# Kernel optimization log

Measured on AMD Instinct MI355X. Metric: run time of the kernel, lower is better.

The kernel has to match this reference:

```python
import jax, jax.numpy as jnp
import numpy as np
from jax import lax

# norse LIFParameters defaults: dt=1e-3, tau_mem_inv=100, tau_syn_inv=200, v_leak=0, v_reset=0
ALPHA = 100.0
DT_TM = 0.1   # dt * tau_mem_inv
DT_TS = 0.2   # dt * tau_syn_inv

@jax.custom_vjp
def superspike(x):
    # Heaviside forward, SuperSpike surrogate gradient backward
    return (x > 0).astype(x.dtype)

def _ss_fwd(x):
    return superspike(x), x

def _ss_bwd(x, g):
    return (g / (ALPHA * jnp.abs(x) + 1.0) ** 2,)

superspike.defvjp(_ss_fwd, _ss_bwd)

def lif_step(inp, v, i, v_th):
    # norse lif_feed_forward_step (feedforward LIF cell)
    v_dec = v + DT_TM * (i - v)           # v_leak = 0
    i_dec = i * (1.0 - DT_TS)
    z = superspike(v_dec - v_th)
    v_new = (1.0 - z) * v_dec             # reset to v_reset = 0 on spike
    return z, v_new, i_dec + inp

def conv2d(x, w):
    return lax.conv_general_dilated(x, w, (1, 1), 'VALID',
                                    dimension_numbers=('NCHW', 'OIHW', 'NCHW'))

def avg_pool2(x):
    s = lax.reduce_window(x, jnp.zeros((), x.dtype), lax.add,
                          (1, 1, 2, 2), (1, 1, 2, 2), 'VALID')
    return s * jnp.asarray(0.25, x.dtype)

def setup_inputs() -> dict:
    key = jax.random.key(0)
    ks = jax.random.split(key, 6)
    x = jax.random.uniform(ks[0], (40, 256, 1, 28, 28), dtype=jnp.float32)
    # kaiming-ish scales (1/sqrt(fan_in))
    w_conv1 = jax.random.normal(ks[1], (20, 1, 3, 3), jnp.float32) * (1.0 / np.sqrt(9))
    w_conv2 = jax.random.normal(ks[2], (50, 20, 3, 3), jnp.float32) * (1.0 / np.sqrt(180))
    w_fc1 = jax.random.normal(ks[3], (500, 6050), jnp.float32) * (1.0 / np.sqrt(6050))
    w_fc2 = jax.random.normal(ks[4], (200, 500), jnp.float32) * (1.0 / np.sqrt(500))
    w_fc_out = jax.random.normal(ks[5], (10, 200), jnp.float32) * (1.0 / np.sqrt(200))
    return {"x": x, "w_conv1": w_conv1, "w_conv2": w_conv2,
            "w_fc1": w_fc1, "w_fc2": w_fc2, "w_fc_out": w_fc_out}

def reference(x, w_conv1, w_conv2, w_fc1, w_fc2, w_fc_out):
    T, B = x.shape[0], x.shape[1]
    dt = x.dtype
    z0 = jnp.zeros((B, 20, 26, 26), dt)
    z1 = jnp.zeros((B, 50, 11, 11), dt)
    z2 = jnp.zeros((B, 500), dt)
    z3 = jnp.zeros((B, 200), dt)
    zo = jnp.zeros((B, 10), dt)
    carry0 = (z0, z0, z1, z1, z2, z2, z3, z3, zo, zo)

    def step(carry, xt):
        v0, i0, v1, i1, v2, i2, v3, i3, vo, io = carry
        z = conv2d(xt, w_conv1)
        z, v0, i0 = lif_step(z, v0, i0, 0.2)
        z = avg_pool2(z)
        z = conv2d(z, w_conv2)
        z, v1, i1 = lif_step(z, v1, i1, 0.2)
        z = z.reshape(B, -1)                      # [B, 50*11*11]
        z = z @ w_fc1.T
        z, v2, i2 = lif_step(z, v2, i2, 0.1)
        z = z @ w_fc2.T
        z, v3, i3 = lif_step(z, v3, i3, 0.05)
        z = z @ w_fc_out.T
        # LICell (norse li_feed_forward_step): output is decayed membrane voltage
        v_dec = vo + DT_TM * (io - vo)
        i_new = io * (1.0 - DT_TS) + z
        return (v0, i0, v1, i1, v2, i2, v3, i3, v_dec, i_new), v_dec

    _, voltages = lax.scan(step, carry0, x)
    return voltages  # [T, B, output_neurons]
```

## Files before the change

kernel.cpp:

```cpp
#include <hip/hip_runtime.h>
#include <hip/hip_bf16.h>

typedef _Float16 f16x8 __attribute__((ext_vector_type(8)));
typedef float f32x4  __attribute__((ext_vector_type(4)));
typedef unsigned short u16x4 __attribute__((ext_vector_type(4)));

#define T_STEPS 40
#define BATCH   256
#define S2LO    0.000244140625f

__device__ __forceinline__ unsigned short f2h_bits(float f) {
    union { _Float16 h; unsigned short u; } c; c.h = (_Float16)f; return c.u;
}

__device__ __forceinline__ float lif_update(float inp, float& v, float& i, float vth) {
    float vd = __fadd_rn(v, __fmul_rn(0.1f, __fsub_rn(i, v)));
    float id = __fmul_rn(0.8f, i);
    float z  = (vd > vth) ? 1.0f : 0.0f;
    v = (vd > vth) ? 0.0f : vd;
    i = __fadd_rn(id, inp);
    return z;
}

__device__ __forceinline__ void llds16(const unsigned short* g, void* l) {
    __builtin_amdgcn_global_load_lds(
        (const __attribute__((address_space(1))) unsigned int*)g,
        (__attribute__((address_space(3))) unsigned int*)l, 16, 0, 0);
}

__global__ __launch_bounds__(512) void k_conv1(
    const float* __restrict__ x,
    const float* __restrict__ w1,
    unsigned char* __restrict__ s0)
{
    const int b    = blockIdx.y;
    const int tid  = threadIdx.x;
    const int cell = blockIdx.x*512 + tid;
    const bool active = cell < 3380;
    const int pos  = cell / 20;
    const int oc   = cell % 20;
    const int pr   = pos / 13, q = pos % 13;
    const int r0   = 2*pr, c0 = 2*q;

    __shared__ __align__(16) float xl[2][784];

    float wr[9];
    if (active) {
        #pragma unroll
        for (int j = 0; j < 9; ++j) wr[j] = w1[oc*9 + j];
    }
    float vs[2][2], is[2][2];
    #pragma unroll
    for (int dr = 0; dr < 2; ++dr)
        #pragma unroll
        for (int dc = 0; dc < 2; ++dc) { vs[dr][dc] = 0.f; is[dr][dc] = 0.f; }

    if (tid < 196) {
        const float4* xs4 = (const float4*)(x + (size_t)b*784);
        *(float4*)&xl[0][tid*4] = xs4[tid];
    }

    for (int t = 0; t < T_STEPS; ++t) {
        __syncthreads();
        if (t + 1 < T_STEPS && tid < 196) {
            const float4* xs4 = (const float4*)(x + (size_t)((t+1)*BATCH + b)*784);
            *(float4*)&xl[(t+1)&1][tid*4] = xs4[tid];
        }
        const float* xc = xl[t&1];
        size_t base = (size_t)(t*BATCH + b) * 4096;

        if (active) {
            float tle[4][4];
            #pragma unroll
            for (int r = 0; r < 4; ++r) {
                *(float2*)&tle[r][0] = *(const float2*)&xc[(r0 + r)*28 + c0];
                *(float2*)&tle[r][2] = *(const float2*)&xc[(r0 + r)*28 + c0 + 2];
            }
            int zsum = 0;
            #pragma unroll
            for (int dr = 0; dr < 2; ++dr)
                #pragma unroll
                for (int dc = 0; dc < 2; ++dc) {
                    float acc = 0.f;
                    #pragma unroll
                    for (int kr = 0; kr < 3; ++kr)
                        #pragma unroll
                        for (int kc = 0; kc < 3; ++kc)
                            acc += tle[dr+kr][dc+kc] * wr[kr*3+kc];
                    float z = lif_update(acc, vs[dr][dc], is[dr][dc], 0.2f);
                    zsum += (z > 0.5f) ? 1 : 0;
                }
            s0[base + (size_t)pos*24 + oc] = (unsigned char)zsum;
        } else {
            int p2 = cell - 3380;
            for (int idx = p2; idx < 716; idx += 204) {
                if (idx < 676) s0[base + (size_t)(idx >> 2)*24 + 20 + (idx & 3)] = 0;
                else           s0[base + 4056 + (idx - 676)] = 0;
            }
        }
    }
}

__global__ __launch_bounds__(256, 2) void k_conv2(
    const unsigned char* __restrict__ s0,
    const float* __restrict__ w2,
    unsigned short* __restrict__ z1)
{
    const int b    = blockIdx.x >> 1;
    const int half = blockIdx.x & 1;
    const int tid  = threadIdx.x;
    const int wv   = tid >> 6;
    const int lane = tid & 63;
    const int l15  = lane & 15;
    const int kg   = lane >> 4;
    const int wm   = wv;

    __shared__ __align__(16) unsigned short w2h[32*232];
    __shared__ __align__(16) unsigned short w2m[32*232];
    __shared__ __align__(16) unsigned short sIn[2*4096];

    for (int s = tid; s < 32*232; s += 256) {
        int ocw = s / 232, kk = s % 232;
        int g = kk / 24, ic = kk % 24;
        int oc = half*32 + ocw;
        float val = 0.f;
        if (oc < 50 && g < 9 && ic < 20) val = w2[(oc*20 + ic)*9 + g];
        _Float16 h = (_Float16)val;
        float r1 = (val - (float)h) * 4096.0f;
        union { _Float16 h; unsigned short u; } ch, cm;
        ch.h = h; cm.h = (_Float16)r1;
        w2h[s] = ch.u;
        w2m[s] = cm.u;
    }

    int addrA[2][7];
    #pragma unroll
    for (int mt = 0; mt < 2; ++mt) {
        int pos = wm*32 + mt*16 + l15;
        #pragma unroll
        for (int kt = 0; kt < 7; ++kt) {
            int k = kt*32 + kg*8;
            int g = k / 24, o = k - g*24;
            if (pos <= 120 && g <= 8) {
                int in_idx = pos + 2*(pos/11) + 13*(g/3) + (g % 3);
                addrA[mt][kt] = in_idx*48 + o*2;
            } else addrA[mt][kt] = 8128;
        }
    }

    {
        const unsigned char* srow = s0 + (size_t)(0*BATCH + b)*4096;
        uint4 raw = *(const uint4*)(srow + tid*16);
        unsigned short hv[16];
        #pragma unroll
        for (int w = 0; w < 4; ++w) {
            unsigned int u = ((const unsigned int*)&raw)[w];
            #pragma unroll
            for (int j = 0; j < 4; ++j)
                hv[w*4+j] = f2h_bits(0.25f * (float)((u >> (8*j)) & 0xFFu));
        }
        unsigned short* dst = sIn + tid*16;
        *(f16x8*)dst       = *(const f16x8*)&hv[0];
        *(f16x8*)(dst + 8) = *(const f16x8*)&hv[8];
    }
    __syncthreads();

    f16x8 bfrH[2][7], bfrM[2][7];
    #pragma unroll
    for (int nt = 0; nt < 2; ++nt) {
        int n = nt*16 + l15;
        #pragma unroll
        for (int kt = 0; kt < 7; ++kt) {
            bfrH[nt][kt] = *(const f16x8*)&w2h[n*232 + kt*32 + kg*8];
            bfrM[nt][kt] = *(const f16x8*)&w2m[n*232 + kt*32 + kg*8];
        }
    }

    float vst[2][2][4], ist[2][2][4];
    #pragma unroll
    for (int mt = 0; mt < 2; ++mt)
        #pragma unroll
        for (int nt = 0; nt < 2; ++nt)
            #pragma unroll
            for (int r = 0; r < 4; ++r) { vst[mt][nt][r] = 0.f; ist[mt][nt][r] = 0.f; }

    const f32x4 zero4 = {0.f, 0.f, 0.f, 0.f};

    for (int t = 0; t < T_STEPS; ++t) {
        if (t > 0) __syncthreads();

        uint4 raw;
        if (t + 1 < T_STEPS)
            raw = *(const uint4*)(s0 + (size_t)((t+1)*BATCH + b)*4096 + tid*16);

        const char* curB = (const char*)(sIn + (t&1)*4096);

        f32x4 acch[2][2], accl[2][2];
        #pragma unroll
        for (int mt = 0; mt < 2; ++mt)
            #pragma unroll
            for (int nt = 0; nt < 2; ++nt) { acch[mt][nt] = zero4; accl[mt][nt] = zero4; }

        #pragma unroll
        for (int kt = 0; kt < 7; ++kt) {
            #pragma unroll
            for (int mt = 0; mt < 2; ++mt) {
                f16x8 a = *(const f16x8*)(curB + addrA[mt][kt]);
                #pragma unroll
                for (int nt = 0; nt < 2; ++nt) {
                    acch[mt][nt] = __builtin_amdgcn_mfma_f32_16x16x32_f16(
                        a, bfrH[nt][kt], acch[mt][nt], 0, 0, 0);
                    accl[mt][nt] = __builtin_amdgcn_mfma_f32_16x16x32_f16(
                        a, bfrM[nt][kt], accl[mt][nt], 0, 0, 0);
                }
            }
        }

        size_t rowoff = (size_t)(t*BATCH + b) * 6208;
        #pragma unroll
        for (int mt = 0; mt < 2; ++mt) {
            int posb = wm*32 + mt*16 + kg*4;
            #pragma unroll
            for (int nt = 0; nt < 2; ++nt) {
                int ocn = half*32 + nt*16 + l15;
                u16x4 pack;
                #pragma unroll
                for (int r = 0; r < 4; ++r) {
                    float inp = __fadd_rn(acch[mt][nt][r], __fmul_rn(S2LO, accl[mt][nt][r]));
                    float z = lif_update(inp, vst[mt][nt][r], ist[mt][nt][r], 0.2f);
                    int pos = posb + r;
                    pack[r] = (pos <= 120 && z > 0.5f) ? (unsigned short)0x3C00 : (unsigned short)0;
                }
                if (ocn < 50 && posb < 121)
                    *(u16x4*)(z1 + rowoff + ocn*124 + posb) = pack;
            }
        }
        if (half == 0 && tid < 8) z1[rowoff + 6200 + tid] = 0;

        if (t + 1 < T_STEPS) {
            unsigned short hv[16];
            #pragma unroll
            for (int w = 0; w < 4; ++w) {
                unsigned int u = ((const unsigned int*)&raw)[w];
                #pragma unroll
                for (int j = 0; j < 4; ++j)
                    hv[w*4+j] = f2h_bits(0.25f * (float)((u >> (8*j)) & 0xFFu));
            }
            unsigned short* dst = sIn + ((t+1)&1)*4096 + tid*16;
            *(f16x8*)dst       = *(const f16x8*)&hv[0];
            *(f16x8*)(dst + 8) = *(const f16x8*)&hv[8];
        }
    }
}

__global__ __launch_bounds__(256, 3) void k_gemm(
    const unsigned short* __restrict__ A,
    const unsigned short* __restrict__ B0,
    float* __restrict__ C0,
    int Kp, int kiters, int ldc, int nstore,
    size_t strideB, size_t strideC)
{
    __shared__ __align__(16) unsigned short As[128*64];
    __shared__ __align__(16) unsigned short Bs[128*64];
    const unsigned short* B = B0 + (size_t)blockIdx.z * strideB;
    float* C = C0 + (size_t)blockIdx.z * strideC;

    const int tid  = threadIdx.x;
    const int lane = tid & 63;
    const int wv   = tid >> 6;
    const int wm   = wv & 1, wn = wv >> 1;
    const int l15  = lane & 15, kg = lane >> 4;
    const int mbase = blockIdx.x * 128;
    const int nbase = blockIdx.y * 128;

    const f32x4 zero4 = {0.f, 0.f, 0.f, 0.f};
    f32x4 acc[4][4];
    #pragma unroll
    for (int mt = 0; mt < 4; ++mt)
        #pragma unroll
        for (int nt = 0; nt < 4; ++nt) acc[mt][nt] = zero4;

    const int rowA = tid >> 3;
    const int sw   = (((tid & 7) ^ (rowA & 7))) * 8;
    char* ldsA = (char*)As + (size_t)wv*1024;
    char* ldsB = (char*)Bs + (size_t)wv*1024;

    for (int ki = 0; ki < kiters; ++ki) {
        int kb = ki * 64;
        #pragma unroll
        for (int c = 0; c < 4; ++c) {
            int row = c*32 + rowA;
            llds16(A + (size_t)(mbase + row)*Kp + kb + sw, ldsA + c*4096);
            llds16(B + (size_t)(nbase + row)*Kp + kb + sw, ldsB + c*4096);
        }
        __syncthreads();
        #pragma unroll
        for (int kt = 0; kt < 2; ++kt) {
            f16x8 bfv[4], afv[4];
            #pragma unroll
            for (int nt = 0; nt < 4; ++nt) {
                int rb = wn*64 + nt*16 + l15;
                int ch = ((kt*4 + kg) ^ (rb & 7)) * 8;
                bfv[nt] = *(const f16x8*)&Bs[rb*64 + ch];
            }
            #pragma unroll
            for (int mt = 0; mt < 4; ++mt) {
                int ra = wm*64 + mt*16 + l15;
                int ch = ((kt*4 + kg) ^ (ra & 7)) * 8;
                afv[mt] = *(const f16x8*)&As[ra*64 + ch];
            }
            #pragma unroll
            for (int mt = 0; mt < 4; ++mt)
                #pragma unroll
                for (int nt = 0; nt < 4; ++nt)
                    acc[mt][nt] = __builtin_amdgcn_mfma_f32_16x16x32_f16(
                        afv[mt], bfv[nt], acc[mt][nt], 0, 0, 0);
        }
        __syncthreads();
    }

    #pragma unroll
    for (int mt = 0; mt < 4; ++mt) {
        int m0 = mbase + wm*64 + mt*16 + kg*4;
        #pragma unroll
        for (int nt = 0; nt < 4; ++nt) {
            int n = nbase + wn*64 + nt*16 + l15;
            if (n < nstore) {
                #pragma unroll
                for (int r = 0; r < 4; ++r)
                    C[(size_t)(m0 + r)*ldc + n] = acc[mt][nt][r];
            }
        }
    }
}

__global__ void k_pack_all(const float* __restrict__ wf1, const float* __restrict__ wf2,
                           const float* __restrict__ wfo,
                           unsigned short* __restrict__ W1, unsigned short* __restrict__ W2,
                           unsigned short* __restrict__ Wo) {
    int idx = blockIdx.x*256 + threadIdx.x;
    float v; unsigned short *hi, *lo; int off;
    if (idx < 3178496) {
        int n = idx / 6208, k = idx - n*6208;
        int oc = k / 124, pos = k - oc*124;
        v = (n < 500 && oc < 50 && pos < 121) ? wf1[n*6050 + oc*121 + pos] : 0.f;
        hi = W1; lo = W1 + 3178496; off = idx;
    } else if (idx < 3178496 + 131072) {
        int i2 = idx - 3178496;
        int n = i2 / 512, k = i2 - n*512;
        v = (n < 200 && k < 500) ? wf2[n*500 + k] : 0.f;
        hi = W2; lo = W2 + 131072; off = i2;
    } else if (idx < 3178496 + 131072 + 32768) {
        int i3 = idx - 3178496 - 131072;
        int n = i3 / 256, k = i3 - n*256;
        v = (n < 10 && k < 200) ? wfo[n*200 + k] : 0.f;
        hi = Wo; lo = Wo + 32768; off = i3;
    } else return;
    _Float16 h = (_Float16)v;
    float r1 = (v - (float)h) * 4096.0f;
    union { _Float16 h; unsigned short u; } ch, cl;
    ch.h = h; cl.h = (_Float16)r1;
    hi[off] = ch.u;
    lo[off] = cl.u;
}

__global__ __launch_bounds__(512) void k_lif_scan(
    const float* __restrict__ c0, size_t pstride,
    unsigned short* __restrict__ zout,
    int ld, int nvalid, float vth)
{
    int b = blockIdx.x;
    int n = threadIdx.x;
    float v = 0.f, cur = 0.f;
    size_t idx0 = (size_t)b*ld + n;
    float hi = c0[idx0], lo = c0[idx0 + pstride];
    for (int t = 0; t < T_STEPS; ++t) {
        float nhi = 0.f, nlo = 0.f;
        if (t + 1 < T_STEPS) {
            size_t nidx = (size_t)((t+1)*BATCH + b)*ld + n;
            nhi = c0[nidx]; nlo = c0[nidx + pstride];
        }
        float s = __fadd_rn(hi, __fmul_rn(S2LO, lo));
        float z = lif_update(s, v, cur, vth);
        zout[(size_t)(t*BATCH + b)*ld + n] =
            (n < nvalid && z > 0.5f) ? (unsigned short)0x3C00 : (unsigned short)0;
        hi = nhi; lo = nlo;
    }
}

__global__ void k_li(const float* __restrict__ c0, size_t pstride, float* __restrict__ out) {
    int g = blockIdx.x*64 + threadIdx.x;
    if (g >= 2560) return;
    int b = g / 10, n = g - b*10;
    float vo = 0.f, io = 0.f;
    for (int t = 0; t < T_STEPS; ++t) {
        size_t idx = (size_t)(t*BATCH + b)*16 + n;
        float s = __fadd_rn(c0[idx], __fmul_rn(S2LO, c0[idx + pstride]));
        float vd = __fadd_rn(vo, __fmul_rn(0.1f, __fsub_rn(io, vo)));
        out[(size_t)(t*BATCH + b)*10 + n] = vd;
        io = __fadd_rn(__fmul_rn(0.8f, io), s);
        vo = vd;
    }
}

extern "C" void kernel_launch(void* const* d_in, const int* in_sizes, int n_in,
                              void* d_out, int out_size, void* d_ws, size_t ws_size,
                              hipStream_t stream) {
    (void)in_sizes; (void)n_in; (void)out_size; (void)ws_size;
    const float* x   = (const float*)d_in[0];
    const float* w1  = (const float*)d_in[1];
    const float* w2  = (const float*)d_in[2];
    const float* wf1 = (const float*)d_in[3];
    const float* wf2 = (const float*)d_in[4];
    const float* wfo = (const float*)d_in[5];
    char* ws = (char*)d_ws;

    unsigned short* z1    = (unsigned short*)(ws);
    unsigned char*  s0    = (unsigned char*)(ws + 127139840);
    unsigned short* W1hi  = (unsigned short*)(ws + 127139840);
    unsigned short* W2hi  = (unsigned short*)(ws + 139853824);
    unsigned short* Wohi  = (unsigned short*)(ws + 140378112);
    float*          c2p   = (float*)(ws + 140509184);
    unsigned short* z2    = (unsigned short*)(ws);
    float*          c3p   = (float*)(ws + 10485760);
    unsigned short* z3    = (unsigned short*)(ws + 31457280);
    float*          c4p   = (float*)(ws + 36700160);

    k_conv1<<<dim3(7, 256), 512, 0, stream>>>(x, w1, s0);
    k_conv2<<<512, 256, 0, stream>>>(s0, w2, z1);

    k_pack_all<<<(3342336+255)/256, 256, 0, stream>>>(wf1, wf2, wfo, W1hi, W2hi, Wohi);

    k_gemm<<<dim3(80,4,2), 256, 0, stream>>>(z1, W1hi, c2p, 6208, 97, 512, 512,
                                             (size_t)3178496, (size_t)5242880);
    k_lif_scan<<<256, 512, 0, stream>>>(c2p, (size_t)5242880, z2, 512, 500, 0.1f);
    k_gemm<<<dim3(80,2,2), 256, 0, stream>>>(z2, W2hi, c3p, 512, 8, 256, 256,
                                             (size_t)131072, (size_t)2621440);
    k_lif_scan<<<256, 256, 0, stream>>>(c3p, (size_t)2621440, z3, 256, 200, 0.05f);
    k_gemm<<<dim3(80,1,2), 256, 0, stream>>>(z3, Wohi, c4p, 256, 4, 16, 16,
                                             (size_t)32768, (size_t)163840);
    k_li<<<40, 64, 0, stream>>>(c4p, (size_t)163840, (float*)d_out);
}
```

Before: 405.5 us.

## Fuse conv1 LIF and conv2 into one kernel keeping spikes in LDS

Merges the conv1+LIF+pool kernel with the conv2 MFMA kernel into one per-batch block of 512 threads. Pooled conv1 spike counts now stay in shared memory as fp16 instead of going through a global byte buffer. Each thread handles up to 7 pooled positions with their LIF state held in registers, and conv2 weights are reloaded from LDS every step rather than kept in registers. This removes a kernel launch and the global round-trip for s0. The cost is fewer blocks (256 vs 512+1792), only one block per CU, and conv1 and conv2 running serially inside each timestep.

```diff
diff --git a/kernel.cpp b/kernel.cpp
--- a/kernel.cpp
+++ b/kernel.cpp
@@ -28,101 +28,29 @@
         (__attribute__((address_space(3))) unsigned int*)l, 16, 0, 0);
 }
 
-__global__ __launch_bounds__(512) void k_conv1(
+__global__ __launch_bounds__(512, 1) void k_conv_fused(
     const float* __restrict__ x,
     const float* __restrict__ w1,
-    unsigned char* __restrict__ s0)
-{
-    const int b    = blockIdx.y;
-    const int tid  = threadIdx.x;
-    const int cell = blockIdx.x*512 + tid;
-    const bool active = cell < 3380;
-    const int pos  = cell / 20;
-    const int oc   = cell % 20;
-    const int pr   = pos / 13, q = pos % 13;
-    const int r0   = 2*pr, c0 = 2*q;
-
-    __shared__ __align__(16) float xl[2][784];
-
-    float wr[9];
-    if (active) {
-        #pragma unroll
-        for (int j = 0; j < 9; ++j) wr[j] = w1[oc*9 + j];
-    }
-    float vs[2][2], is[2][2];
-    #pragma unroll
-    for (int dr = 0; dr < 2; ++dr)
-        #pragma unroll
-        for (int dc = 0; dc < 2; ++dc) { vs[dr][dc] = 0.f; is[dr][dc] = 0.f; }
-
-    if (tid < 196) {
-        const float4* xs4 = (const float4*)(x + (size_t)b*784);
-        *(float4*)&xl[0][tid*4] = xs4[tid];
-    }
-
-    for (int t = 0; t < T_STEPS; ++t) {
-        __syncthreads();
-        if (t + 1 < T_STEPS && tid < 196) {
-            const float4* xs4 = (const float4*)(x + (size_t)((t+1)*BATCH + b)*784);
-            *(float4*)&xl[(t+1)&1][tid*4] = xs4[tid];
-        }
-        const float* xc = xl[t&1];
-        size_t base = (size_t)(t*BATCH + b) * 4096;
-
-        if (active) {
-            float tle[4][4];
-            #pragma unroll
-            for (int r = 0; r < 4; ++r) {
-                *(float2*)&tle[r][0] = *(const float2*)&xc[(r0 + r)*28 + c0];
-                *(float2*)&tle[r][2] = *(const float2*)&xc[(r0 + r)*28 + c0 + 2];
-            }
-            int zsum = 0;
-            #pragma unroll
-            for (int dr = 0; dr < 2; ++dr)
-                #pragma unroll
-                for (int dc = 0; dc < 2; ++dc) {
-                    float acc = 0.f;
-                    #pragma unroll
-                    for (int kr = 0; kr < 3; ++kr)
-                        #pragma unroll
-                        for (int kc = 0; kc < 3; ++kc)
-                            acc += tle[dr+kr][dc+kc] * wr[kr*3+kc];
-                    float z = lif_update(acc, vs[dr][dc], is[dr][dc], 0.2f);
-                    zsum += (z > 0.5f) ? 1 : 0;
-                }
-            s0[base + (size_t)pos*24 + oc] = (unsigned char)zsum;
-        } else {
-            int p2 = cell - 3380;
-            for (int idx = p2; idx < 716; idx += 204) {
-                if (idx < 676) s0[base + (size_t)(idx >> 2)*24 + 20 + (idx & 3)] = 0;
-                else           s0[base + 4056 + (idx - 676)] = 0;
-            }
-        }
-    }
-}
-
-__global__ __launch_bounds__(256, 2) void k_conv2(
-    const unsigned char* __restrict__ s0,
     const float* __restrict__ w2,
     unsigned short* __restrict__ z1)
 {
-    const int b    = blockIdx.x >> 1;
-    const int half = blockIdx.x & 1;
+    const int b    = blockIdx.x;
     const int tid  = threadIdx.x;
     const int wv   = tid >> 6;
     const int lane = tid & 63;
     const int l15  = lane & 15;
     const int kg   = lane >> 4;
-    const int wm   = wv;
-
-    __shared__ __align__(16) unsigned short w2h[32*232];
-    __shared__ __align__(16) unsigned short w2m[32*232];
-    __shared__ __align__(16) unsigned short sIn[2*4096];
-
-    for (int s = tid; s < 32*232; s += 256) {
-        int ocw = s / 232, kk = s % 232;
+    const int wm   = wv & 3;
+    const int wn   = wv >> 2;
+
+    __shared__ __align__(16) float xl[2][784];
+    __shared__ __align__(16) unsigned short s0l[200*24];
+    __shared__ __align__(16) unsigned short w2h[64*232];
+    __shared__ __align__(16) unsigned short w2m[64*232];
+
+    for (int s = tid; s < 64*232; s += 512) {
+        int oc = s / 232, kk = s % 232;
         int g = kk / 24, ic = kk % 24;
-        int oc = half*32 + ocw;
         float val = 0.f;
         if (oc < 50 && g < 9 && ic < 20) val = w2[(oc*20 + ic)*9 + g];
         _Float16 h = (_Float16)val;
@@ -132,6 +60,23 @@
         w2h[s] = ch.u;
         w2m[s] = cm.u;
     }
+    for (int s = tid; s < 4800; s += 512) s0l[s] = 0;
+
+    const bool c1act = tid < 500;
+    const int oc1 = tid % 20;
+    const int pg  = tid / 20;
+    float wr[9];
+    if (c1act) {
+        #pragma unroll
+        for (int j = 0; j < 9; ++j) wr[j] = w1[oc1*9 + j];
+    }
+    float vs[7][2][2], is[7][2][2];
+    #pragma unroll
+    for (int j = 0; j < 7; ++j)
+        #pragma unroll
+        for (int dr = 0; dr < 2; ++dr)
+            #pragma unroll
+            for (int dc = 0; dc < 2; ++dc) { vs[j][dr][dc] = 0.f; is[j][dr][dc] = 0.f; }
 
     int addrA[2][7];
     #pragma unroll
@@ -147,71 +92,87 @@
             } else addrA[mt][kt] = 8128;
         }
     }
-
-    {
-        const unsigned char* srow = s0 + (size_t)(0*BATCH + b)*4096;
-        uint4 raw = *(const uint4*)(srow + tid*16);
-        unsigned short hv[16];
-        #pragma unroll
-        for (int w = 0; w < 4; ++w) {
-            unsigned int u = ((const unsigned int*)&raw)[w];
-            #pragma unroll
-            for (int j = 0; j < 4; ++j)
-                hv[w*4+j] = f2h_bits(0.25f * (float)((u >> (8*j)) & 0xFFu));
-        }
-        unsigned short* dst = sIn + tid*16;
-        *(f16x8*)dst       = *(const f16x8*)&hv[0];
-        *(f16x8*)(dst + 8) = *(const f16x8*)&hv[8];
+    float vst[2][2][4], ist[2][2][4];
+    #pragma unroll
+    for (int mt = 0; mt < 2; ++mt)
+        #pragma unroll
+        for (int nt = 0; nt < 2; ++nt)
+            #pragma unroll
+            for (int r = 0; r < 4; ++r) { vst[mt][nt][r] = 0.f; ist[mt][nt][r] = 0.f; }
+
+    if (tid < 196) {
+        *(float4*)&xl[0][tid*4] = ((const float4*)(x + (size_t)b*784))[tid];
     }
     __syncthreads();
 
-    f16x8 bfrH[2][7], bfrM[2][7];
-    #pragma unroll
-    for (int nt = 0; nt < 2; ++nt) {
-        int n = nt*16 + l15;
+    const f32x4 zero4 = {0.f, 0.f, 0.f, 0.f};
+    const char* s0lB = (const char*)s0l;
+
+    for (int t = 0; t < T_STEPS; ++t) {
+        float4 xnext;
+        if (t + 1 < T_STEPS && tid < 196)
+            xnext = ((const float4*)(x + (size_t)((t+1)*BATCH + b)*784))[tid];
+
+        const float* xc = xl[t&1];
+        if (c1act) {
+            #pragma unroll
+            for (int j = 0; j < 7; ++j) {
+                int pos = pg + 25*j;
+                bool act = (j < 6) || (pos < 169);
+                int posc = act ? pos : 0;
+                int pr = posc / 13, q = posc % 13;
+                int r0 = 2*pr, c0 = 2*q;
+                float tle[4][4];
+                #pragma unroll
+                for (int r = 0; r < 4; ++r) {
+                    *(float2*)&tle[r][0] = *(const float2*)&xc[(r0 + r)*28 + c0];
+                    *(float2*)&tle[r][2] = *(const float2*)&xc[(r0 + r)*28 + c0 + 2];
+                }
+                int zsum = 0;
+                #pragma unroll
+                for (int dr = 0; dr < 2; ++dr)
+                    #pragma unroll
+                    for (int dc = 0; dc < 2; ++dc) {
+                        float acc = 0.f;
+                        #pragma unroll
+                        for (int kr = 0; kr < 3; ++kr)
+                            #pragma unroll
+                            for (int kc = 0; kc < 3; ++kc)
+                                acc += tle[dr+kr][dc+kc] * wr[kr*3+kc];
+                        float z = lif_update(acc, vs[j][dr][dc], is[j][dr][dc], 0.2f);
+                        zsum += (z > 0.5f) ? 1 : 0;
+                    }
+                if (act)
+                    s0l[posc*24 + oc1] = f2h_bits(0.25f * (float)zsum);
+            }
+        }
+        __syncthreads();
+
+        f32x4 acch[2][2], accl[2][2];
+        #pragma unroll
+        for (int mt = 0; mt < 2; ++mt)
+            #pragma unroll
+            for (int nt = 0; nt < 2; ++nt) { acch[mt][nt] = zero4; accl[mt][nt] = zero4; }
+
         #pragma unroll
         for (int kt = 0; kt < 7; ++kt) {
-            bfrH[nt][kt] = *(const f16x8*)&w2h[n*232 + kt*32 + kg*8];
-            bfrM[nt][kt] = *(const f16x8*)&w2m[n*232 + kt*32 + kg*8];
-        }
-    }
-
-    float vst[2][2][4], ist[2][2][4];
-    #pragma unroll
-    for (int mt = 0; mt < 2; ++mt)
-        #pragma unroll
-        for (int nt = 0; nt < 2; ++nt)
-            #pragma unroll
-            for (int r = 0; r < 4; ++r) { vst[mt][nt][r] = 0.f; ist[mt][nt][r] = 0.f; }
-
-    const f32x4 zero4 = {0.f, 0.f, 0.f, 0.f};
-
-    for (int t = 0; t < T_STEPS; ++t) {
-        if (t > 0) __syncthreads();
-
-        uint4 raw;
-        if (t + 1 < T_STEPS)
-            raw = *(const uint4*)(s0 + (size_t)((t+1)*BATCH + b)*4096 + tid*16);
-
-        const char* curB = (const char*)(sIn + (t&1)*4096);
-
-        f32x4 acch[2][2], accl[2][2];
-        #pragma unroll
-        for (int mt = 0; mt < 2; ++mt)
-            #pragma unroll
-            for (int nt = 0; nt < 2; ++nt) { acch[mt][nt] = zero4; accl[mt][nt] = zero4; }
-
-        #pragma unroll
-        for (int kt = 0; kt < 7; ++kt) {
+            f16x8 bh[2], bm[2];
+            #pragma unroll
+            for (int nt = 0; nt < 2; ++nt) {
+                int n = wn*32 + nt*16 + l15;
+                int k = kt*32 + kg*8;
+                bh[nt] = *(const f16x8*)&w2h[n*232 + k];
+                bm[nt] = *(const f16x8*)&w2m[n*232 + k];
+            }
             #pragma unroll
             for (int mt = 0; mt < 2; ++mt) {
-                f16x8 a = *(const f16x8*)(curB + addrA[mt][kt]);
+                f16x8 a = *(const f16x8*)(s0lB + addrA[mt][kt]);
                 #pragma unroll
                 for (int nt = 0; nt < 2; ++nt) {
                     acch[mt][nt] = __builtin_amdgcn_mfma_f32_16x16x32_f16(
-                        a, bfrH[nt][kt], acch[mt][nt], 0, 0, 0);
+                        a, bh[nt], acch[mt][nt], 0, 0, 0);
                     accl[mt][nt] = __builtin_amdgcn_mfma_f32_16x16x32_f16(
-                        a, bfrM[nt][kt], accl[mt][nt], 0, 0, 0);
+                        a, bm[nt], accl[mt][nt], 0, 0, 0);
                 }
             }
         }
@@ -222,7 +183,7 @@
             int posb = wm*32 + mt*16 + kg*4;
             #pragma unroll
             for (int nt = 0; nt < 2; ++nt) {
-                int ocn = half*32 + nt*16 + l15;
+                int ocn = wn*32 + nt*16 + l15;
                 u16x4 pack;
                 #pragma unroll
                 for (int r = 0; r < 4; ++r) {
@@ -235,21 +196,11 @@
                     *(u16x4*)(z1 + rowoff + ocn*124 + posb) = pack;
             }
         }
-        if (half == 0 && tid < 8) z1[rowoff + 6200 + tid] = 0;
-
-        if (t + 1 < T_STEPS) {
-            unsigned short hv[16];
-            #pragma unroll
-            for (int w = 0; w < 4; ++w) {
-                unsigned int u = ((const unsigned int*)&raw)[w];
-                #pragma unroll
-                for (int j = 0; j < 4; ++j)
-                    hv[w*4+j] = f2h_bits(0.25f * (float)((u >> (8*j)) & 0xFFu));
-            }
-            unsigned short* dst = sIn + ((t+1)&1)*4096 + tid*16;
-            *(f16x8*)dst       = *(const f16x8*)&hv[0];
-            *(f16x8*)(dst + 8) = *(const f16x8*)&hv[8];
-        }
+        if (tid < 8) z1[rowoff + 6200 + tid] = 0;
+
+        if (t + 1 < T_STEPS && tid < 196)
+            *(float4*)&xl[(t+1)&1][tid*4] = xnext;
+        __syncthreads();
     }
 }
 
@@ -416,7 +367,6 @@
     char* ws = (char*)d_ws;
 
     unsigned short* z1    = (unsigned short*)(ws);
-    unsigned char*  s0    = (unsigned char*)(ws + 127139840);
     unsigned short* W1hi  = (unsigned short*)(ws + 127139840);
     unsigned short* W2hi  = (unsigned short*)(ws + 139853824);
     unsigned short* Wohi  = (unsigned short*)(ws + 140378112);
@@ -426,8 +376,7 @@
     unsigned short* z3    = (unsigned short*)(ws + 31457280);
     float*          c4p   = (float*)(ws + 36700160);
 
-    k_conv1<<<dim3(7, 256), 512, 0, stream>>>(x, w1, s0);
-    k_conv2<<<512, 256, 0, stream>>>(s0, w2, z1);
+    k_conv_fused<<<256, 512, 0, stream>>>(x, w1, w2, z1);
 
     k_pack_all<<<(3342336+255)/256, 256, 0, stream>>>(wf1, wf2, wfo, W1hi, W2hi, Wohi);
 
```

New measurement: 742.7 us. +83.2%, slower.
